# Optimization experiments

Hardware: AMD Instinct MI355X
Metric: run time of the kernel (lower is better)

The kernel has to match this reference:

```python
import jax, jax.numpy as jnp
import numpy as np

PATCH = 32          # feature map is PATCH x PATCH, N = PATCH**2 tokens
HEADS = 8
HD = 24             # head_dim (hardcoded in Block -> Cluster3D)
P = 4               # proposal_w = proposal_h = 4 -> 16 cluster centers
EPS_NORM = 1e-12    # F.normalize eps
LN_EPS = 1e-5


def _layernorm(x, g, b):
    m = x.mean(-1, keepdims=True)
    v = ((x - m) ** 2).mean(-1, keepdims=True)
    return (x - m) / jnp.sqrt(v + LN_EPS) * g + b


def _cluster3d(xn, f_w, f_b, v_w, v_b, alpha, beta, proj_w, proj_b):
    # xn: [B, N, D] with tokens laid out row-major over a PATCH x PATCH grid
    B, N, D = xn.shape
    M = P * P
    feat = xn @ f_w.T + f_b   # [B, N, HEADS*HD]  (1x1 conv f)
    val = xn @ v_w.T + v_b    # [B, N, HEADS*HD]  (1x1 conv v)

    def to_heads(t):  # channel layout is (e c): head-major
        return t.reshape(B, N, HEADS, HD).transpose(0, 2, 1, 3).reshape(B * HEADS, N, HD)

    fh = to_heads(feat)       # [Bh, N, HD]
    vh = to_heads(val)

    def pool(t):  # AdaptiveAvgPool to (P, P) over the PATCH x PATCH grid
        g = t.reshape(-1, P, PATCH // P, P, PATCH // P, HD).mean(axis=(2, 4))
        return g.reshape(-1, M, HD)

    centers = pool(fh)        # [Bh, M, HD]
    vcenters = pool(vh)       # [Bh, M, HD]

    cn = centers / jnp.clip(jnp.linalg.norm(centers, axis=-1, keepdims=True), EPS_NORM)
    fn = fh / jnp.clip(jnp.linalg.norm(fh, axis=-1, keepdims=True), EPS_NORM)
    sim = beta + alpha * jnp.einsum('bmc,bnc->bmn', cn, fn)   # [Bh, M, N]
    sim = jnp.where(sim >= 0, sim, 0.2 * sim)                 # LeakyReLU(0.2); dropout eval=identity

    # hard top-1 assignment of each token to its best center
    idx = jnp.argmax(sim, axis=1)                              # [Bh, N]
    mask = jax.nn.one_hot(idx, M, dtype=sim.dtype).transpose(0, 2, 1)  # [Bh, M, N]
    mask = jax.lax.stop_gradient(mask)
    sim = sim * mask

    # aggregate tokens into centers, then dispatch back
    agg = (jnp.einsum('bmn,bnc->bmc', sim, vh) + vcenters) / (mask.sum(-1, keepdims=True) + 1.0)
    out = jnp.einsum('bmn,bmc->bnc', sim, agg)                 # [Bh, N, HD]

    out = out.reshape(B, HEADS, N, HD).transpose(0, 2, 1, 3).reshape(B, N, HEADS * HD)
    return out @ proj_w.T + proj_b                             # [B, N, D]


def setup_inputs() -> dict:
    key = jax.random.key(0)
    ks = jax.random.split(key, 8)
    B, N, D, HID, HH = 64, PATCH * PATCH, 512, 2048, HEADS * HD
    s = 0.02
    return {
        'x': jax.random.normal(ks[0], (B, N, D), jnp.float32),
        'ln1_g': jnp.ones((D,), jnp.float32),
        'ln1_b': jnp.zeros((D,), jnp.float32),
        'f_w': jax.random.normal(ks[1], (HH, D), jnp.float32) * s,
        'f_b': jnp.zeros((HH,), jnp.float32),
        'v_w': jax.random.normal(ks[2], (HH, D), jnp.float32) * s,
        'v_b': jnp.zeros((HH,), jnp.float32),
        'sim_alpha': jnp.ones((1,), jnp.float32),
        'sim_beta': jnp.zeros((1,), jnp.float32),
        'proj_w': jax.random.normal(ks[3], (D, HH), jnp.float32) * s,
        'proj_b': jnp.zeros((D,), jnp.float32),
        'ln2_g': jnp.ones((D,), jnp.float32),
        'ln2_b': jnp.zeros((D,), jnp.float32),
        'fc1_w': jax.random.normal(ks[4], (HID, D), jnp.float32) * s,
        'fc1_b': jnp.zeros((HID,), jnp.float32),
        'fc2_w': jax.random.normal(ks[5], (D, HID), jnp.float32) * s,
        'fc2_b': jnp.zeros((D,), jnp.float32),
    }


def reference(x, ln1_g, ln1_b, f_w, f_b, v_w, v_b, sim_alpha, sim_beta,
              proj_w, proj_b, ln2_g, ln2_b, fc1_w, fc1_b, fc2_w, fc2_b):
    x = x + _cluster3d(_layernorm(x, ln1_g, ln1_b), f_w, f_b, v_w, v_b,
                       sim_alpha, sim_beta, proj_w, proj_b)
    h = _layernorm(x, ln2_g, ln2_b)
    h = jax.nn.gelu(h @ fc1_w.T + fc1_b, approximate=False)
    x = x + (h @ fc2_w.T + fc2_b)
    return x
```

## Files before the change

### kernel.cpp

```cpp
#include <hip/hip_runtime.h>


typedef __attribute__((ext_vector_type(8))) short short8;
typedef __attribute__((ext_vector_type(4))) short short4v;
typedef __attribute__((ext_vector_type(4))) float floatx4;

static __device__ __forceinline__ short f2bf(float f) {
  union { float f; unsigned u; } a; a.f = f;
  unsigned r = a.u + 0x7fffu + ((a.u >> 16) & 1u);
  return (short)(r >> 16);
}

static __device__ __forceinline__ void gload_lds16(const short* g, short* l) {
  __builtin_amdgcn_global_load_lds(
      (const __attribute__((address_space(1))) void*)g,
      (__attribute__((address_space(3))) void*)l, 16, 0, 0);
}

__global__ __launch_bounds__(256) void cvt_f32_bf16(
    const float* __restrict__ in, short* __restrict__ out, int n4)
{
  int i = blockIdx.x * 256 + threadIdx.x;
  if (i >= n4) return;
  float4 v = reinterpret_cast<const float4*>(in)[i];
  short4v o;
  o[0] = f2bf(v.x); o[1] = f2bf(v.y); o[2] = f2bf(v.z); o[3] = f2bf(v.w);
  reinterpret_cast<short4v*>(out)[i] = o;
}

__global__ __launch_bounds__(256) void ln_kernel(
    const float* __restrict__ x, const float* __restrict__ g,
    const float* __restrict__ b, short* __restrict__ out)
{
  const int wave = threadIdx.x >> 6, lane = threadIdx.x & 63;
  const size_t row = (size_t)blockIdx.x * 4 + wave;
  const float* xr = x + row * 512;
  const int c = lane * 8;
  float4 v0 = *reinterpret_cast<const float4*>(xr + c);
  float4 v1 = *reinterpret_cast<const float4*>(xr + c + 4);
  float xs[8] = {v0.x, v0.y, v0.z, v0.w, v1.x, v1.y, v1.z, v1.w};
  float s = 0.f, q = 0.f;
#pragma unroll
  for (int k = 0; k < 8; ++k) { s += xs[k]; q += xs[k] * xs[k]; }
#pragma unroll
  for (int off = 32; off; off >>= 1) {
    s += __shfl_xor(s, off);
    q += __shfl_xor(q, off);
  }
  const float mean = s * (1.0f / 512.0f);
  const float var  = q * (1.0f / 512.0f) - mean * mean;
  const float rstd = rsqrtf(var + 1e-5f);
  short8 o;
#pragma unroll
  for (int k = 0; k < 8; ++k)
    o[k] = f2bf((xs[k] - mean) * rstd * g[c + k] + b[c + k]);
  *reinterpret_cast<short8*>(out + row * 512 + c) = o;
}

template<int BM, int BN, int WM, int WN, int EPI>
__global__ __launch_bounds__(256, 2) void gemm_bt(
    const short* __restrict__ A, const short* __restrict__ W,
    const float* __restrict__ bias, const float* __restrict__ resid,
    float* __restrict__ Cf, short* __restrict__ Cb,
    const int N, const int K)
{
  constexpr int BK = 32;
  constexpr int T  = 256;
  constexpr int AC = (BM * BK / 8) / T;
  constexpr int WC = (BN * BK / 8) / T;
  __shared__ short Al[2][BM * BK];
  __shared__ short Wl[2][BN * BK];
  const int tid  = threadIdx.x;
  const int wave = tid >> 6;
  const int lane = tid & 63;
  constexpr int WCOLS = BN / WN;
  const int wm = (wave / WCOLS) * WM;
  const int wn = (wave % WCOLS) * WN;
  constexpr int MI = WM / 16, NJ = WN / 16;
  const int row0 = blockIdx.x * BM;
  const int col0 = blockIdx.y * BN;
  const int r  = lane & 15;
  const int kc = lane >> 4;

  floatx4 acc[MI][NJ];
#pragma unroll
  for (int i = 0; i < MI; ++i)
#pragma unroll
    for (int j = 0; j < NJ; ++j)
      acc[i][j] = (floatx4){0.f, 0.f, 0.f, 0.f};

  const short* Ab = A + (size_t)row0 * K;
  const short* Wb = W + (size_t)col0 * K;

  const short* aSrc[AC]; int aDst[AC];
#pragma unroll
  for (int u = 0; u < AC; ++u) {
    const int cc = u * T + tid;
    const int rr = cc >> 2, sl = cc & 3;
    const int co = sl ^ ((rr >> 1) & 3);
    aSrc[u] = Ab + (size_t)rr * K + co * 8;
    aDst[u] = cc * 8;
  }
  const short* wSrc[WC]; int wDst[WC];
#pragma unroll
  for (int u = 0; u < WC; ++u) {
    const int cc = u * T + tid;
    const int rr = cc >> 2, sl = cc & 3;
    const int co = sl ^ ((rr >> 1) & 3);
    wSrc[u] = Wb + (size_t)rr * K + co * 8;
    wDst[u] = cc * 8;
  }
  int aOff[MI], wOff[NJ];
#pragma unroll
  for (int i = 0; i < MI; ++i) {
    const int rt = wm + 16 * i + r;
    aOff[i] = rt * BK + ((kc ^ ((rt >> 1) & 3)) << 3);
  }
#pragma unroll
  for (int j = 0; j < NJ; ++j) {
    const int rt = wn + 16 * j + r;
    wOff[j] = rt * BK + ((kc ^ ((rt >> 1) & 3)) << 3);
  }

  auto stage = [&](int buf, int k0) {
#pragma unroll
    for (int u = 0; u < AC; ++u) gload_lds16(aSrc[u] + k0, &Al[buf][aDst[u]]);
#pragma unroll
    for (int u = 0; u < WC; ++u) gload_lds16(wSrc[u] + k0, &Wl[buf][wDst[u]]);
  };

  stage(0, 0);
  __syncthreads();
  int cur = 0;
  for (int k0 = BK; k0 <= K; k0 += BK) {
    if (k0 < K) stage(cur ^ 1, k0);
    short8 af[MI], wfr[NJ];
#pragma unroll
    for (int i = 0; i < MI; ++i)
      af[i] = *reinterpret_cast<const short8*>(&Al[cur][aOff[i]]);
#pragma unroll
    for (int j = 0; j < NJ; ++j)
      wfr[j] = *reinterpret_cast<const short8*>(&Wl[cur][wOff[j]]);
#pragma unroll
    for (int i = 0; i < MI; ++i)
#pragma unroll
      for (int j = 0; j < NJ; ++j)
        acc[i][j] = __builtin_amdgcn_mfma_f32_16x16x32_bf16(
            af[i], wfr[j], acc[i][j], 0, 0, 0);
    __syncthreads();
    cur ^= 1;
  }

#pragma unroll
  for (int i = 0; i < MI; ++i) {
#pragma unroll
    for (int j = 0; j < NJ; ++j) {
      const int col = col0 + wn + 16 * j + r;
      const float bv = bias[col];
#pragma unroll
      for (int t = 0; t < 4; ++t) {
        const int rowi = row0 + wm + 16 * i + (lane >> 4) * 4 + t;
        const size_t offo = (size_t)rowi * N + col;
        float v = acc[i][j][t] + bv;
        if (EPI == 0) {
          Cf[offo] = v;
        } else if (EPI == 1) {
          Cf[offo] = v + resid[offo];
        } else {
          v = 0.5f * v * (1.0f + erff(v * 0.70710678118654752f));
          Cb[offo] = f2bf(v);
        }
      }
    }
  }
}

template<int EPI>
__global__ __launch_bounds__(512, 1) void gemm512(
    const short* __restrict__ A, const short* __restrict__ W,
    const float* __restrict__ bias, const float* __restrict__ resid,
    float* __restrict__ Cf, short* __restrict__ Cb,
    const int N, const int K)
{
  constexpr int BM = 256, BN = 256, BK = 32;
  constexpr int T  = 512;
  constexpr int AC = (BM * BK / 8) / T;
  constexpr int WC = (BN * BK / 8) / T;
  constexpr int WM = 128, WN = 64;
  constexpr int MI = WM / 16, NJ = WN / 16;
  __shared__ short Al[2][BM * BK];
  __shared__ short Wl[2][BN * BK];
  const int tid  = threadIdx.x;
  const int wave = tid >> 6;
  const int lane = tid & 63;
  const int wm = (wave >> 2) * WM;
  const int wn = (wave & 3) * WN;
  const int row0 = blockIdx.x * BM;
  const int col0 = blockIdx.y * BN;
  const int r  = lane & 15;
  const int kc = lane >> 4;

  floatx4 acc[MI][NJ];
#pragma unroll
  for (int i = 0; i < MI; ++i)
#pragma unroll
    for (int j = 0; j < NJ; ++j)
      acc[i][j] = (floatx4){0.f, 0.f, 0.f, 0.f};

  const short* Ab = A + (size_t)row0 * K;
  const short* Wb = W + (size_t)col0 * K;

  const short* aSrc[AC]; int aDst[AC];
#pragma unroll
  for (int u = 0; u < AC; ++u) {
    const int cc = u * T + tid;
    const int rr = cc >> 2, sl = cc & 3;
    const int co = sl ^ ((rr >> 1) & 3);
    aSrc[u] = Ab + (size_t)rr * K + co * 8;
    aDst[u] = cc * 8;
  }
  const short* wSrc[WC]; int wDst[WC];
#pragma unroll
  for (int u = 0; u < WC; ++u) {
    const int cc = u * T + tid;
    const int rr = cc >> 2, sl = cc & 3;
    const int co = sl ^ ((rr >> 1) & 3);
    wSrc[u] = Wb + (size_t)rr * K + co * 8;
    wDst[u] = cc * 8;
  }
  int aOff[MI], wOff[NJ];
#pragma unroll
  for (int i = 0; i < MI; ++i) {
    const int rt = wm + 16 * i + r;
    aOff[i] = rt * BK + ((kc ^ ((rt >> 1) & 3)) << 3);
  }
#pragma unroll
  for (int j = 0; j < NJ; ++j) {
    const int rt = wn + 16 * j + r;
    wOff[j] = rt * BK + ((kc ^ ((rt >> 1) & 3)) << 3);
  }

  auto stage = [&](int buf, int k0) {
#pragma unroll
    for (int u = 0; u < AC; ++u) gload_lds16(aSrc[u] + k0, &Al[buf][aDst[u]]);
#pragma unroll
    for (int u = 0; u < WC; ++u) gload_lds16(wSrc[u] + k0, &Wl[buf][wDst[u]]);
  };

  stage(0, 0);
  __syncthreads();
  int cur = 0;
  for (int k0 = BK; k0 <= K; k0 += BK) {
    if (k0 < K) stage(cur ^ 1, k0);
    short8 af[MI], wfr[NJ];
#pragma unroll
    for (int i = 0; i < MI; ++i)
      af[i] = *reinterpret_cast<const short8*>(&Al[cur][aOff[i]]);
#pragma unroll
    for (int j = 0; j < NJ; ++j)
      wfr[j] = *reinterpret_cast<const short8*>(&Wl[cur][wOff[j]]);
#pragma unroll
    for (int i = 0; i < MI; ++i)
#pragma unroll
      for (int j = 0; j < NJ; ++j)
        acc[i][j] = __builtin_amdgcn_mfma_f32_16x16x32_bf16(
            af[i], wfr[j], acc[i][j], 0, 0, 0);
    __syncthreads();
    cur ^= 1;
  }

#pragma unroll
  for (int i = 0; i < MI; ++i) {
#pragma unroll
    for (int j = 0; j < NJ; ++j) {
      const int col = col0 + wn + 16 * j + r;
      const float bv = bias[col];
#pragma unroll
      for (int t = 0; t < 4; ++t) {
        const int rowi = row0 + wm + 16 * i + kc * 4 + t;
        const size_t offo = (size_t)rowi * N + col;
        float v = acc[i][j][t] + bv;
        if (EPI == 1) {
          Cf[offo] = v + resid[offo];
        } else {
          v = 0.5f * v * (1.0f + erff(v * 0.70710678118654752f));
          Cb[offo] = f2bf(v);
        }
      }
    }
  }
}

__global__ __launch_bounds__(384) void pool_kernel(
    const float* __restrict__ feat, const float* __restrict__ val,
    float* __restrict__ cn, float* __restrict__ vcent)
{
  const int bh = blockIdx.x;
  const int b = bh >> 3, h = bh & 7;
  const int t = threadIdx.x;
  const int m = t / 24, c = t % 24;
  const int cy = m >> 2, cx = m & 3;
  const size_t base = (size_t)b * 1024 * 192 + h * 24 + c;
  float sf = 0.f, sv = 0.f;
  for (int dy = 0; dy < 8; ++dy) {
    const int ny = (cy * 8 + dy) * 32 + cx * 8;
    for (int dx = 0; dx < 8; ++dx) {
      const size_t off = base + (size_t)(ny + dx) * 192;
      sf += feat[off];
      sv += val[off];
    }
  }
  sf *= (1.0f / 64.0f); sv *= (1.0f / 64.0f);
  __shared__ float cent[16][24];
  cent[m][c] = sf;
  vcent[(size_t)bh * 384 + t] = sv;
  __syncthreads();
  float nrm = 0.f;
#pragma unroll
  for (int k = 0; k < 24; ++k) nrm += cent[m][k] * cent[m][k];
  nrm = fmaxf(sqrtf(nrm), 1e-12f);
  cn[(size_t)bh * 384 + t] = sf / nrm;
}

__global__ __launch_bounds__(256) void sim_kernel(
    const float* __restrict__ feat, const float* __restrict__ cn,
    const float* __restrict__ alpha_p, const float* __restrict__ beta_p,
    float* __restrict__ sval, int* __restrict__ sidx)
{
  const int bh = blockIdx.y;
  const int b = bh >> 3, h = bh & 7;
  __shared__ float cs[384];
  for (int i = threadIdx.x; i < 384; i += 256) cs[i] = cn[(size_t)bh * 384 + i];
  __syncthreads();
  const int n = blockIdx.x * 256 + threadIdx.x;
  const float* f = feat + (size_t)(b * 1024 + n) * 192 + h * 24;
  float v[24];
#pragma unroll
  for (int k = 0; k < 24; k += 4) {
    float4 t4 = *reinterpret_cast<const float4*>(f + k);
    v[k] = t4.x; v[k + 1] = t4.y; v[k + 2] = t4.z; v[k + 3] = t4.w;
  }
  float q = 0.f;
#pragma unroll
  for (int k = 0; k < 24; ++k) q += v[k] * v[k];
  const float inv = 1.0f / fmaxf(sqrtf(q), 1e-12f);
  const float alpha = alpha_p[0], beta = beta_p[0];
  float best = -3.4e38f; int bi = 0;
#pragma unroll
  for (int m = 0; m < 16; ++m) {
    float d = 0.f;
#pragma unroll
    for (int k = 0; k < 24; ++k) d += cs[m * 24 + k] * v[k];
    float s = beta + alpha * (d * inv);
    s = (s < 0.f) ? 0.2f * s : s;
    if (s > best) { best = s; bi = m; }
  }
  sval[(size_t)bh * 1024 + n] = best;
  sidx[(size_t)bh * 1024 + n] = bi;
}

__global__ __launch_bounds__(256) void agg_kernel(
    const float* __restrict__ val, const float* __restrict__ vcent,
    const float* __restrict__ sval, const int* __restrict__ sidx,
    float* __restrict__ agg)
{
  const int bh = blockIdx.x;
  const int b = bh >> 3, h = bh & 7;
  __shared__ float acc[384];
  __shared__ float cnt[16];
  for (int i = threadIdx.x; i < 384; i += 256) acc[i] = 0.f;
  if (threadIdx.x < 16) cnt[threadIdx.x] = 0.f;
  __syncthreads();
  for (int n = threadIdx.x; n < 1024; n += 256) {
    const float s = sval[(size_t)bh * 1024 + n];
    const int m = sidx[(size_t)bh * 1024 + n];
    atomicAdd(&cnt[m], 1.0f);
    const float* vv = val + (size_t)(b * 1024 + n) * 192 + h * 24;
#pragma unroll
    for (int k = 0; k < 24; ++k) atomicAdd(&acc[m * 24 + k], s * vv[k]);
  }
  __syncthreads();
  for (int i = threadIdx.x; i < 384; i += 256) {
    const int m = i / 24;
    agg[(size_t)bh * 384 + i] = (acc[i] + vcent[(size_t)bh * 384 + i]) / (cnt[m] + 1.0f);
  }
}

__global__ __launch_bounds__(256) void dispatch_kernel(
    const float* __restrict__ sval, const int* __restrict__ sidx,
    const float* __restrict__ agg, short* __restrict__ o)
{
  const int g = blockIdx.x * 256 + threadIdx.x;
  const int h = g & 7, n = (g >> 3) & 1023, b = g >> 13;
  const int bh = b * 8 + h;
  const float s = sval[(size_t)bh * 1024 + n];
  const int m = sidx[(size_t)bh * 1024 + n];
  const float* a = agg + (size_t)bh * 384 + m * 24;
  short* op = o + ((size_t)(b * 1024 + n)) * 192 + h * 24;
  short8 pack[3];
#pragma unroll
  for (int k = 0; k < 24; ++k) pack[k >> 3][k & 7] = f2bf(s * a[k]);
  short8* dst = reinterpret_cast<short8*>(op);
  dst[0] = pack[0]; dst[1] = pack[1]; dst[2] = pack[2];
}

extern "C" void kernel_launch(void* const* d_in, const int* in_sizes, int n_in,
                              void* d_out, int out_size, void* d_ws, size_t ws_size,
                              hipStream_t stream)
{
  const float* x      = (const float*)d_in[0];
  const float* ln1_g  = (const float*)d_in[1];
  const float* ln1_b  = (const float*)d_in[2];
  const float* f_w    = (const float*)d_in[3];
  const float* f_b    = (const float*)d_in[4];
  const float* v_w    = (const float*)d_in[5];
  const float* v_b    = (const float*)d_in[6];
  const float* alpha  = (const float*)d_in[7];
  const float* beta   = (const float*)d_in[8];
  const float* proj_w = (const float*)d_in[9];
  const float* proj_b = (const float*)d_in[10];
  const float* ln2_g  = (const float*)d_in[11];
  const float* ln2_b  = (const float*)d_in[12];
  const float* fc1_w  = (const float*)d_in[13];
  const float* fc1_b  = (const float*)d_in[14];
  const float* fc2_w  = (const float*)d_in[15];
  const float* fc2_b  = (const float*)d_in[16];
  float* out = (float*)d_out;

  char* ws = (char*)d_ws;
  size_t off = 0;
  auto alloc = [&](size_t bytes) -> char* {
    char* p = ws + off;
    off = (off + bytes + 255) & ~(size_t)255;
    return p;
  };
  short* xn   = (short*)alloc(67108864);
  float* feat = (float*)alloc(50331648);
  float* val  = (float*)alloc(50331648);
  short* o    = (short*)alloc(25165824);
  float* x1   = (float*)alloc(134217728);
  short* wf   = (short*)alloc(196608);
  short* wv   = (short*)alloc(196608);
  short* wp   = (short*)alloc(196608);
  short* w1   = (short*)alloc(2097152);
  short* w2   = (short*)alloc(2097152);
  float* cnb  = (float*)alloc(786432);
  float* vcb  = (float*)alloc(786432);
  float* agb  = (float*)alloc(786432);
  float* svb  = (float*)alloc(2097152);
  int*   sib  = (int*)  alloc(2097152);
  short* h  = (short*)feat;

  const size_t h1_bytes = 134217728;
  short* h1;
  int nchunk;
  if (ws_size >= off + h1_bytes) {
    h1 = (short*)alloc(h1_bytes);
    nchunk = 2;
  } else {
    h1 = xn;
    nchunk = 4;
  }
  const int MCH = 65536 / nchunk;

  cvt_f32_bf16<<<96,   256, 0, stream>>>(f_w,    wf, 24576);
  cvt_f32_bf16<<<96,   256, 0, stream>>>(v_w,    wv, 24576);
  cvt_f32_bf16<<<96,   256, 0, stream>>>(proj_w, wp, 24576);
  cvt_f32_bf16<<<1024, 256, 0, stream>>>(fc1_w,  w1, 262144);
  cvt_f32_bf16<<<1024, 256, 0, stream>>>(fc2_w,  w2, 262144);

  ln_kernel<<<16384, 256, 0, stream>>>(x, ln1_g, ln1_b, xn);

  gemm_bt<256, 64, 64, 64, 0><<<dim3(256, 3), 256, 0, stream>>>(
      xn, wf, f_b, nullptr, feat, nullptr, 192, 512);
  gemm_bt<256, 64, 64, 64, 0><<<dim3(256, 3), 256, 0, stream>>>(
      xn, wv, v_b, nullptr, val, nullptr, 192, 512);

  pool_kernel<<<512, 384, 0, stream>>>(feat, val, cnb, vcb);
  sim_kernel<<<dim3(4, 512), 256, 0, stream>>>(feat, cnb, alpha, beta, svb, sib);
  agg_kernel<<<512, 256, 0, stream>>>(val, vcb, svb, sib, agb);
  dispatch_kernel<<<2048, 256, 0, stream>>>(svb, sib, agb, o);

  gemm_bt<128, 128, 64, 64, 1><<<dim3(512, 4), 256, 0, stream>>>(
      o, wp, proj_b, x, x1, nullptr, 512, 192);

  ln_kernel<<<16384, 256, 0, stream>>>(x1, ln2_g, ln2_b, h);

  for (int c = 0; c < nchunk; ++c) {
    const short* hA = h + (size_t)c * MCH * 512;
    gemm512<2><<<dim3(MCH / 256, 8), 512, 0, stream>>>(
        hA, w1, fc1_b, nullptr, nullptr, h1, 2048, 512);
    gemm512<1><<<dim3(MCH / 256, 2), 512, 0, stream>>>(
        h1, w2, fc2_b, x1 + (size_t)c * MCH * 512,
        out + (size_t)c * MCH * 512, nullptr, 512, 2048);
  }
  (void)in_sizes; (void)n_in; (void)out_size;
}
```

Measured before the change: 1.184 ms.

## Triple-buffer MLP GEMM loads with explicit waitcnt and allow single-chunk MLP

The 256x256 MLP GEMM moves from double-buffered static LDS to a three-stage dynamic-LDS pipeline. Loads run three tiles ahead, with partial vmcnt waits, raw barriers, sched_barriers and setprio around the MFMA block, so global-to-LDS latency is hidden better. The workspace logic can also allocate a full 256MB h1 buffer so the MLP runs as one chunk, which cuts launches. If the dynamic shared-memory attribute cannot be set, the code falls back to gemm_bt. The cost is more LDS per block and correctness that depends on hand-placed wait counts.

After: 1.003 ms. -15.3%, faster.

```diff
diff --git a/kernel.cpp b/kernel.cpp
--- a/kernel.cpp
+++ b/kernel.cpp
@@ -176,110 +176,109 @@
 }
 
 template<int EPI>
-__global__ __launch_bounds__(512, 1) void gemm512(
+__global__ __launch_bounds__(512, 1) void gemm_deep(
     const short* __restrict__ A, const short* __restrict__ W,
     const float* __restrict__ bias, const float* __restrict__ resid,
     float* __restrict__ Cf, short* __restrict__ Cb,
     const int N, const int K)
 {
   constexpr int BM = 256, BN = 256, BK = 32;
-  constexpr int T  = 512;
-  constexpr int AC = (BM * BK / 8) / T;
-  constexpr int WC = (BN * BK / 8) / T;
-  constexpr int WM = 128, WN = 64;
-  constexpr int MI = WM / 16, NJ = WN / 16;
-  __shared__ short Al[2][BM * BK];
-  __shared__ short Wl[2][BN * BK];
+  constexpr int BUF = BM * BK;
+  extern __shared__ short lds[];
   const int tid  = threadIdx.x;
   const int wave = tid >> 6;
   const int lane = tid & 63;
-  const int wm = (wave >> 2) * WM;
-  const int wn = (wave & 3) * WN;
+  const int wm = (wave >> 2) * 128;
+  const int wn = (wave & 3) * 64;
   const int row0 = blockIdx.x * BM;
   const int col0 = blockIdx.y * BN;
   const int r  = lane & 15;
   const int kc = lane >> 4;
 
-  floatx4 acc[MI][NJ];
-#pragma unroll
-  for (int i = 0; i < MI; ++i)
-#pragma unroll
-    for (int j = 0; j < NJ; ++j)
+  floatx4 acc[8][4];
+#pragma unroll
+  for (int i = 0; i < 8; ++i)
+#pragma unroll
+    for (int j = 0; j < 4; ++j)
       acc[i][j] = (floatx4){0.f, 0.f, 0.f, 0.f};
 
   const short* Ab = A + (size_t)row0 * K;
   const short* Wb = W + (size_t)col0 * K;
 
-  const short* aSrc[AC]; int aDst[AC];
-#pragma unroll
-  for (int u = 0; u < AC; ++u) {
-    const int cc = u * T + tid;
+  const short* aSrc[2]; const short* wSrc[2]; int dstO[2];
+#pragma unroll
+  for (int u = 0; u < 2; ++u) {
+    const int cc = u * 512 + tid;
     const int rr = cc >> 2, sl = cc & 3;
     const int co = sl ^ ((rr >> 1) & 3);
     aSrc[u] = Ab + (size_t)rr * K + co * 8;
-    aDst[u] = cc * 8;
-  }
-  const short* wSrc[WC]; int wDst[WC];
-#pragma unroll
-  for (int u = 0; u < WC; ++u) {
-    const int cc = u * T + tid;
-    const int rr = cc >> 2, sl = cc & 3;
-    const int co = sl ^ ((rr >> 1) & 3);
     wSrc[u] = Wb + (size_t)rr * K + co * 8;
-    wDst[u] = cc * 8;
-  }
-  int aOff[MI], wOff[NJ];
-#pragma unroll
-  for (int i = 0; i < MI; ++i) {
+    dstO[u] = cc * 8;
+  }
+  int aOff[8], wOff[4];
+#pragma unroll
+  for (int i = 0; i < 8; ++i) {
     const int rt = wm + 16 * i + r;
     aOff[i] = rt * BK + ((kc ^ ((rt >> 1) & 3)) << 3);
   }
 #pragma unroll
-  for (int j = 0; j < NJ; ++j) {
+  for (int j = 0; j < 4; ++j) {
     const int rt = wn + 16 * j + r;
     wOff[j] = rt * BK + ((kc ^ ((rt >> 1) & 3)) << 3);
   }
 
   auto stage = [&](int buf, int k0) {
-#pragma unroll
-    for (int u = 0; u < AC; ++u) gload_lds16(aSrc[u] + k0, &Al[buf][aDst[u]]);
-#pragma unroll
-    for (int u = 0; u < WC; ++u) gload_lds16(wSrc[u] + k0, &Wl[buf][wDst[u]]);
+    short* base = lds + buf * (2 * BUF);
+#pragma unroll
+    for (int u = 0; u < 2; ++u) gload_lds16(aSrc[u] + k0, base + dstO[u]);
+#pragma unroll
+    for (int u = 0; u < 2; ++u) gload_lds16(wSrc[u] + k0, base + BUF + dstO[u]);
   };
 
+  const int nt = K / BK;
   stage(0, 0);
-  __syncthreads();
+  stage(1, BK);
+  stage(2, 2 * BK);
   int cur = 0;
-  for (int k0 = BK; k0 <= K; k0 += BK) {
-    if (k0 < K) stage(cur ^ 1, k0);
-    short8 af[MI], wfr[NJ];
-#pragma unroll
-    for (int i = 0; i < MI; ++i)
-      af[i] = *reinterpret_cast<const short8*>(&Al[cur][aOff[i]]);
-#pragma unroll
-    for (int j = 0; j < NJ; ++j)
-      wfr[j] = *reinterpret_cast<const short8*>(&Wl[cur][wOff[j]]);
-#pragma unroll
-    for (int i = 0; i < MI; ++i)
-#pragma unroll
-      for (int j = 0; j < NJ; ++j)
+  for (int t = 0; t < nt; ++t) {
+    asm volatile("s_waitcnt vmcnt(8)" ::: "memory");
+    __builtin_amdgcn_s_barrier();
+    __builtin_amdgcn_sched_barrier(0);
+    const short* base = lds + cur * (2 * BUF);
+    short8 af[8], wf[4];
+#pragma unroll
+    for (int i = 0; i < 8; ++i)
+      af[i] = *reinterpret_cast<const short8*>(base + aOff[i]);
+#pragma unroll
+    for (int j = 0; j < 4; ++j)
+      wf[j] = *reinterpret_cast<const short8*>(base + BUF + wOff[j]);
+    asm volatile("s_waitcnt lgkmcnt(0)" ::: "memory");
+    __builtin_amdgcn_sched_barrier(0);
+    __builtin_amdgcn_s_setprio(1);
+#pragma unroll
+    for (int i = 0; i < 8; ++i)
+#pragma unroll
+      for (int j = 0; j < 4; ++j)
         acc[i][j] = __builtin_amdgcn_mfma_f32_16x16x32_bf16(
-            af[i], wfr[j], acc[i][j], 0, 0, 0);
-    __syncthreads();
-    cur ^= 1;
-  }
-
-#pragma unroll
-  for (int i = 0; i < MI; ++i) {
-#pragma unroll
-    for (int j = 0; j < NJ; ++j) {
+            af[i], wf[j], acc[i][j], 0, 0, 0);
+    __builtin_amdgcn_s_setprio(0);
+    __builtin_amdgcn_sched_barrier(0);
+    __builtin_amdgcn_s_barrier();
+    if (t + 3 < nt) stage(cur, (t + 3) * BK);
+    cur = (cur == 2) ? 0 : cur + 1;
+  }
+
+#pragma unroll
+  for (int i = 0; i < 8; ++i) {
+#pragma unroll
+    for (int j = 0; j < 4; ++j) {
       const int col = col0 + wn + 16 * j + r;
       const float bv = bias[col];
 #pragma unroll
-      for (int t = 0; t < 4; ++t) {
-        const int rowi = row0 + wm + 16 * i + kc * 4 + t;
+      for (int tt = 0; tt < 4; ++tt) {
+        const int rowi = row0 + wm + 16 * i + kc * 4 + tt;
         const size_t offo = (size_t)rowi * N + col;
-        float v = acc[i][j][t] + bv;
+        float v = acc[i][j][tt] + bv;
         if (EPI == 1) {
           Cf[offo] = v + resid[offo];
         } else {
@@ -451,17 +450,27 @@
   int*   sib  = (int*)  alloc(2097152);
   short* h  = (short*)feat;
 
-  const size_t h1_bytes = 134217728;
   short* h1;
   int nchunk;
-  if (ws_size >= off + h1_bytes) {
-    h1 = (short*)alloc(h1_bytes);
+  if (ws_size >= off + 268435456) {
+    h1 = (short*)alloc(268435456);
+    nchunk = 1;
+  } else if (ws_size >= off + 134217728) {
+    h1 = (short*)alloc(134217728);
     nchunk = 2;
   } else {
     h1 = xn;
     nchunk = 4;
   }
   const int MCH = 65536 / nchunk;
+
+  hipError_t e1 = hipFuncSetAttribute(
+      reinterpret_cast<const void*>(gemm_deep<2>),
+      hipFuncAttributeMaxDynamicSharedMemorySize, 98304);
+  hipError_t e2 = hipFuncSetAttribute(
+      reinterpret_cast<const void*>(gemm_deep<1>),
+      hipFuncAttributeMaxDynamicSharedMemorySize, 98304);
+  const bool deep = (e1 == hipSuccess) && (e2 == hipSuccess) && (MCH % 256 == 0);
 
   cvt_f32_bf16<<<96,   256, 0, stream>>>(f_w,    wf, 24576);
   cvt_f32_bf16<<<96,   256, 0, stream>>>(v_w,    wv, 24576);
@@ -488,11 +497,19 @@
 
   for (int c = 0; c < nchunk; ++c) {
     const short* hA = h + (size_t)c * MCH * 512;
-    gemm512<2><<<dim3(MCH / 256, 8), 512, 0, stream>>>(
-        hA, w1, fc1_b, nullptr, nullptr, h1, 2048, 512);
-    gemm512<1><<<dim3(MCH / 256, 2), 512, 0, stream>>>(
-        h1, w2, fc2_b, x1 + (size_t)c * MCH * 512,
-        out + (size_t)c * MCH * 512, nullptr, 512, 2048);
+    float* x1c = x1 + (size_t)c * MCH * 512;
+    float* outc = out + (size_t)c * MCH * 512;
+    if (deep) {
+      gemm_deep<2><<<dim3(MCH / 256, 8), 512, 98304, stream>>>(
+          hA, w1, fc1_b, nullptr, nullptr, h1, 2048, 512);
+      gemm_deep<1><<<dim3(MCH / 256, 2), 512, 98304, stream>>>(
+          h1, w2, fc2_b, x1c, outc, nullptr, 512, 2048);
+    } else {
+      gemm_bt<128, 128, 64, 64, 2><<<dim3(MCH / 128, 16), 256, 0, stream>>>(
+          hA, w1, fc1_b, nullptr, nullptr, h1, 2048, 512);
+      gemm_bt<128, 128, 64, 64, 1><<<dim3(MCH / 128, 4), 256, 0, stream>>>(
+          h1, w2, fc2_b, x1c, outc, nullptr, 512, 2048);
+    }
   }
   (void)in_sizes; (void)n_in; (void)out_size;
 }
```
